# Kernel tuning notes

Measured on AMD Instinct MI355X. Metric: run time of the kernel, lower is better.

Reference implementation:

```python
import jax, jax.numpy as jnp
import numpy as np

TAPS = 5
DELAY = 3
EPS_POWER = 1e-7   # clamp for inverse power (wpe_one_iteration eps)
EPS_REG = 1e-10    # diagonal loading of the correlation matrix


def setup_inputs() -> dict:
    key = jax.random.key(0)
    ks = jax.random.split(key, 5)
    B, F, C, T = 8, 257, 8, 800
    shp = (B, F, C, T)
    return {
        "data_sep_real": jax.random.normal(ks[0], shp, jnp.float32),
        "data_sep_imag": jax.random.normal(ks[1], shp, jnp.float32),
        "data_mix_real": jax.random.normal(ks[2], shp, jnp.float32),
        "data_mix_imag": jax.random.normal(ks[3], shp, jnp.float32),
        "ilens": jax.random.randint(ks[4], (B,), 1, T + 1, jnp.int32),
    }


def _ytilde(Y, taps, delay):
    # Y: (B,F,C,T) complex -> stacked delayed taps (B,F,taps*C,T)
    # tap k at time t holds Y[..., t - delay - k] (zero-padded past)
    B, F, C, T = Y.shape
    Yp = jnp.pad(Y, ((0, 0), (0, 0), (0, 0), (delay + taps - 1, 0)))
    tilde = jnp.stack(
        [Yp[..., taps - 1 - k: taps - 1 - k + T] for k in range(taps)], axis=2
    )  # (B,F,taps,C,T)
    return tilde.reshape(B, F, taps * C, T)


def _wpe_one_iteration(Y, power, taps, delay):
    # Y: (B,F,C,T) complex, power: (B,F,T) real
    B, F, C, T = Y.shape
    inv_power = 1.0 / jnp.maximum(power, EPS_POWER)          # (B,F,T)
    Yt = _ytilde(Y, taps, delay)                              # (B,F,K,T), K=taps*C
    t0 = delay + taps - 1                                     # correlations use t >= t0
    Ytv = Yt[..., t0:]
    Yv = Y[..., t0:]
    Ytw = Ytv * inv_power[:, :, None, t0:].astype(Y.dtype)
    # R = sum_t w(t) Ytilde(t) Ytilde(t)^H  -> (B,F,K,K)
    R = jnp.einsum('bfat,bfct->bfac', Ytw, jnp.conj(Ytv))
    # P = sum_t w(t) Ytilde(t) Y(t)^H      -> (B,F,K,C)
    P = jnp.einsum('bfat,bfet->bfae', Ytw, jnp.conj(Yv))
    K = taps * C
    R = R + EPS_REG * jnp.eye(K, dtype=R.dtype)
    G = jnp.linalg.solve(R, P)                                # (B,F,K,C)
    # X(t) = Y(t) - G^H Ytilde(t)
    X = Y - jnp.einsum('bfae,bfat->bfet', jnp.conj(G), Yt)
    return X


def reference(data_sep_real, data_sep_imag, data_mix_real, data_mix_imag, ilens):
    # power of separated signal, averaged over channels (use_dnn_mask=False)
    power = jnp.mean(data_sep_real ** 2 + data_sep_imag ** 2, axis=-2)  # (B,F,T)
    Ym = jax.lax.complex(data_mix_real, data_mix_imag)                  # (B,F,C,T)
    X = _wpe_one_iteration(Ym, power, TAPS, DELAY)
    # zero out padded frames: t >= ilens[b]
    t = jnp.arange(X.shape[-1])
    valid = t[None, :] < ilens[:, None]                                 # (B,T)
    X = jnp.where(valid[:, None, None, :], X, 0)
    # return real/imag stacked on last axis: (B,F,C,T,2)
    return jnp.stack([X.real, X.imag], axis=-1)
```

## Files before the change

### kernel.cpp

```cpp
#include <hip/hip_runtime.h>

#define B 8
#define F 257
#define C 8
#define T 800
#define TAPS 5
#define DELAY 3
#define K 40
#define NCOL 48
#define T0 7
#define BF (B*F)

typedef __bf16 bf16x8 __attribute__((ext_vector_type(8)));
typedef __bf16 bf16x4 __attribute__((ext_vector_type(4)));
typedef float f32x4 __attribute__((ext_vector_type(4)));

struct PF { float4 v[3]; };

__global__ __launch_bounds__(256) void power_kernel(const float* __restrict__ sr,
                                                    const float* __restrict__ si,
                                                    float* __restrict__ W) {
    int bf = blockIdx.x;
    const float* srp = sr + (size_t)bf * C * T;
    const float* sip = si + (size_t)bf * C * T;
    int t0 = threadIdx.x * 4;
    if (t0 < T) {
        float s[4] = {0.f, 0.f, 0.f, 0.f};
#pragma unroll
        for (int c = 0; c < C; ++c) {
            float4 a = *(const float4*)(srp + c * T + t0);
            float4 b = *(const float4*)(sip + c * T + t0);
            s[0] = fmaf(a.x, a.x, fmaf(b.x, b.x, s[0]));
            s[1] = fmaf(a.y, a.y, fmaf(b.y, b.y, s[1]));
            s[2] = fmaf(a.z, a.z, fmaf(b.z, b.z, s[2]));
            s[3] = fmaf(a.w, a.w, fmaf(b.w, b.w, s[3]));
        }
        float4 w;
        float* wp = (float*)&w;
#pragma unroll
        for (int e = 0; e < 4; ++e) {
            float v = fmaxf(s[e] * (1.0f / C), 1e-7f);
            wp[e] = (t0 + e < T0) ? 0.f : rsqrtf(v);
        }
        *(float4*)(W + (size_t)bf * T + t0) = w;
    }
}

#define WB 10624

__global__ __launch_bounds__(256, 3) void rp_mfma_kernel(const float* __restrict__ mr,
                                                         const float* __restrict__ mi,
                                                         const float* __restrict__ W,
                                                         float2* __restrict__ Rout,
                                                         float2* __restrict__ Pout) {
    __shared__ __align__(16) unsigned char SH[4 * WB];
    const int lane = threadIdx.x & 63;
    const int wid = threadIdx.x >> 6;
    const int bf = blockIdx.x * 4 + wid;
    unsigned char* base = SH + wid * WB;
    float* sre = (float*)(base + 7680);
    float* sim_ = (float*)(base + 9088);
    float* wsh = (float*)(base + 10496);

    const float* mrp = mr + (size_t)bf * C * T;
    const float* mip = mi + (size_t)bf * C * T;
    const float* Wp  = W  + (size_t)bf * T;

    const int q = lane >> 4, col = lane & 15;
    const int pc = lane >> 3, pg = lane & 7;

    const int PM[6] = {0, 0, 0, 1, 1, 2};
    const int PN[6] = {0, 1, 2, 1, 2, 2};

    f32x4 accRe[6], accIr[6], accRi[6];
#pragma unroll
    for (int p = 0; p < 6; ++p) {
        accRe[p] = (f32x4){0.f, 0.f, 0.f, 0.f};
        accIr[p] = (f32x4){0.f, 0.f, 0.f, 0.f};
        accRi[p] = (f32x4){0.f, 0.f, 0.f, 0.f};
    }

    for (int ks = 0; ks < 25; ++ks) {
        const int tb = ks * 32;

#pragma unroll
        for (int it = 0; it < 3; ++it) {
            int task = lane + it * 64;
            if (task < 160) {
                int pl = task / 80;
                int rem = task - pl * 80;
                int c = rem / 10, grp = rem - c * 10;
                int tg = tb - 8 + grp * 4;
                const float* srcp = pl ? mip : mrp;
                float4 v = make_float4(0.f, 0.f, 0.f, 0.f);
                if (tg >= 0) v = *(const float4*)(srcp + c * T + tg);
                *(float4*)((pl ? sim_ : sre) + c * 44 + grp * 4) = v;
            } else if (task < 168) {
                int grp = task - 160;
                *(float4*)(wsh + grp * 4) = *(const float4*)(Wp + tb + grp * 4);
            }
        }

        {
            int ybase = pc * 44 + pg * 4;
            float yre[12], yim[12];
            float4 r0 = *(const float4*)(sre + ybase);
            float4 r1 = *(const float4*)(sre + ybase + 4);
            float4 r2 = *(const float4*)(sre + ybase + 8);
            float4 i0 = *(const float4*)(sim_ + ybase);
            float4 i1 = *(const float4*)(sim_ + ybase + 4);
            float4 i2 = *(const float4*)(sim_ + ybase + 8);
            yre[0] = r0.x; yre[1] = r0.y; yre[2]  = r0.z; yre[3]  = r0.w;
            yre[4] = r1.x; yre[5] = r1.y; yre[6]  = r1.z; yre[7]  = r1.w;
            yre[8] = r2.x; yre[9] = r2.y; yre[10] = r2.z; yre[11] = r2.w;
            yim[0] = i0.x; yim[1] = i0.y; yim[2]  = i0.z; yim[3]  = i0.w;
            yim[4] = i1.x; yim[5] = i1.y; yim[6]  = i1.z; yim[7]  = i1.w;
            yim[8] = i2.x; yim[9] = i2.y; yim[10] = i2.z; yim[11] = i2.w;
            float4 w4 = *(const float4*)(wsh + pg * 4);
            float wv[4] = {w4.x, w4.y, w4.z, w4.w};
#pragma unroll
            for (int v = 0; v < 6; ++v) {
                int row = (v < 5) ? (v * 8 + pc) : (40 + pc);
                int off = (v < 5) ? (5 - v) : 8;
                bf16x4 zr, zi;
#pragma unroll
                for (int e = 0; e < 4; ++e) {
                    zr[e] = (__bf16)(wv[e] * yre[off + e]);
                    zi[e] = (__bf16)(wv[e] * yim[off + e]);
                }
                *(bf16x4*)(base + row * 80 + pg * 8) = zr;
                *(bf16x4*)(base + 3840 + row * 80 + pg * 8) = zi;
            }
        }

        bf16x8 fr[3], fi[3];
#pragma unroll
        for (int X = 0; X < 3; ++X) {
            fr[X] = *(const bf16x8*)(base + (X * 16 + col) * 80 + q * 16);
            fi[X] = *(const bf16x8*)(base + 3840 + (X * 16 + col) * 80 + q * 16);
        }
#pragma unroll
        for (int p = 0; p < 6; ++p) {
            int mt = PM[p], nt = PN[p];
            accRe[p] = __builtin_amdgcn_mfma_f32_16x16x32_bf16(fr[mt], fr[nt], accRe[p], 0, 0, 0);
            accRe[p] = __builtin_amdgcn_mfma_f32_16x16x32_bf16(fi[mt], fi[nt], accRe[p], 0, 0, 0);
            accIr[p] = __builtin_amdgcn_mfma_f32_16x16x32_bf16(fi[mt], fr[nt], accIr[p], 0, 0, 0);
            accRi[p] = __builtin_amdgcn_mfma_f32_16x16x32_bf16(fr[mt], fi[nt], accRi[p], 0, 0, 0);
        }
    }

    float2* Rp = Rout + (size_t)bf * K * K;
    float2* Pp = Pout + (size_t)bf * K * C;
#pragma unroll
    for (int p = 0; p < 6; ++p) {
        int mt = PM[p], nt = PN[p];
#pragma unroll
        for (int r = 0; r < 4; ++r) {
            int m = mt * 16 + q * 4 + r;
            int n = nt * 16 + col;
            float re = accRe[p][r];
            float im = accIr[p][r] - accRi[p][r];
            if (m < K) {
                if (n < K) {
                    if (m == n) re += 1e-10f;
                    Rp[m * K + n] = make_float2(re, im);
                } else {
                    Pp[m * C + (n - K)] = make_float2(re, im);
                }
            }
            if (mt != nt && m < K && n < K)
                Rp[n * K + m] = make_float2(re, -im);
        }
    }
}

__device__ __forceinline__ float rdlane(float v, int j) {
    return __uint_as_float(__builtin_amdgcn_readlane(__float_as_uint(v), (unsigned)j));
}

__global__ __launch_bounds__(64, 2) void solve_kernel(const float2* __restrict__ Rin,
                                                      const float2* __restrict__ Pin,
                                                      float2* __restrict__ Gout) {
    const int bf = blockIdx.x;
    const int lane = threadIdx.x;
    const bool act = lane < K;

    float2 row[NCOL];
    {
        const float4* Rp4 = (const float4*)(Rin + (size_t)bf * K * K + (size_t)(act ? lane : 0) * K);
        const float4* Pp4 = (const float4*)(Pin + (size_t)bf * K * C + (size_t)(act ? lane : 0) * C);
#pragma unroll
        for (int m = 0; m < K / 2; ++m) {
            float4 v = Rp4[m];
            if (!act) v = make_float4(0.f, 0.f, 0.f, 0.f);
            row[2 * m]     = make_float2(v.x, v.y);
            row[2 * m + 1] = make_float2(v.z, v.w);
        }
#pragma unroll
        for (int m = 0; m < C / 2; ++m) {
            float4 v = Pp4[m];
            if (!act) v = make_float4(0.f, 0.f, 0.f, 0.f);
            row[K + 2 * m]     = make_float2(v.x, v.y);
            row[K + 2 * m + 1] = make_float2(v.z, v.w);
        }
    }

#pragma unroll
    for (int j = 0; j < K; ++j) {
        float dx = rdlane(row[j].x, j);
        float dy = rdlane(row[j].y, j);
        float den = fmaf(dx, dx, dy * dy);
        float r = 1.0f / den;
        float ix = dx * r;
        float iy = -dy * r;
        float lx = row[j].x * ix - row[j].y * iy;
        float ly = row[j].x * iy + row[j].y * ix;
        bool isj = (lane == j);
        lx = isj ? (1.0f - ix) : lx;
        ly = isj ? (0.0f - iy) : ly;
#pragma unroll
        for (int n = j; n < NCOL; ++n) {
            float ux = rdlane(row[n].x, j);
            float uy = rdlane(row[n].y, j);
            row[n].x = fmaf(-lx, ux, fmaf( ly, uy, row[n].x));
            row[n].y = fmaf(-lx, uy, fmaf(-ly, ux, row[n].y));
        }
    }

    if (act) {
        float4* Gp = (float4*)(Gout + (size_t)bf * K * C + (size_t)lane * C);
#pragma unroll
        for (int m = 0; m < C / 2; ++m)
            Gp[m] = make_float4(row[K + 2 * m].x, row[K + 2 * m].y,
                                row[K + 2 * m + 1].x, row[K + 2 * m + 1].y);
    }
}

#define XSTR 144
#define XWB 12032

__device__ __forceinline__ PF x_load(const float* __restrict__ mrp,
                                     const float* __restrict__ mip,
                                     int tb, int lane) {
    PF p;
#pragma unroll
    for (int it = 0; it < 3; ++it) {
        int task = lane + it * 64;
        float4 v = make_float4(0.f, 0.f, 0.f, 0.f);
        if (task < 160) {
            int pl = task / 80;
            int rem = task - pl * 80;
            int c = rem / 10, grp = rem - c * 10;
            int tg = tb - 8 + grp * 4;
            const float* srcp = pl ? mip : mrp;
            if (tg >= 0) v = *(const float4*)(srcp + c * T + tg);
        }
        p.v[it] = v;
    }
    return p;
}

__device__ __forceinline__ void x_store(const PF& p, float* sre, float* sim_, int lane) {
#pragma unroll
    for (int it = 0; it < 3; ++it) {
        int task = lane + it * 64;
        if (task < 160) {
            int pl = task / 80;
            int rem = task - pl * 80;
            int c = rem / 10, grp = rem - c * 10;
            *(float4*)((pl ? sim_ : sre) + c * 44 + grp * 4) = p.v[it];
        }
    }
}

__global__ __launch_bounds__(64) void x_mfma_kernel(const float* __restrict__ mr,
                                                    const float* __restrict__ mi,
                                                    const float2* __restrict__ Gin,
                                                    const int* __restrict__ ilens,
                                                    float2* __restrict__ out) {
    __shared__ __align__(16) unsigned char SH[XWB];
    const int lane = threadIdx.x;
    const int gid = blockIdx.x;
    const int bf = gid >> 2;
    const int split = gid & 3;
    const int ck0 = (split == 0) ? 0 : (1 + split * 6);
    const int nck = (split == 0) ? 7 : 6;
    unsigned char* base = SH;
    float* sre = (float*)(base + 9216);
    float* sim_ = (float*)(base + 10624);

    const float* mrp = mr + (size_t)bf * C * T;
    const float* mip = mi + (size_t)bf * C * T;
    const float2* Gp = Gin + (size_t)bf * K * C;
    float2* outp = out + (size_t)bf * C * T;
    const int len = ilens[bf / F];

    const int q = lane >> 4, col = lane & 15;
    const int t2 = lane >> 1, half = lane & 1;

#pragma unroll
    for (int pl = 0; pl < 2; ++pl) {
        unsigned char* pb = base + pl * 4608 + t2 * XSTR + 80 + half * 24;
        *(float2*)(pb)      = make_float2(0.f, 0.f);
        *(float2*)(pb + 8)  = make_float2(0.f, 0.f);
        *(float2*)(pb + 16) = make_float2(0.f, 0.f);
    }

    bf16x8 Agr[2], Agi[2], Agin[2];
#pragma unroll
    for (int ks = 0; ks < 2; ++ks)
#pragma unroll
        for (int j = 0; j < 8; ++j) {
            int a = ks * 32 + q * 8 + j;
            float2 g = make_float2(0.f, 0.f);
            if (a < K && col < C) g = Gp[a * C + col];
            Agr[ks][j]  = (__bf16)g.x;
            Agi[ks][j]  = (__bf16)g.y;
            Agin[ks][j] = (__bf16)(-g.y);
        }

    PF cur = x_load(mrp, mip, ck0 * 32, lane);

    for (int ci = 0; ci < nck; ++ci) {
        const int tb = (ck0 + ci) * 32;

        x_store(cur, sre, sim_, lane);
        if (ci + 1 < nck) cur = x_load(mrp, mip, tb + 32, lane);

#pragma unroll
        for (int i = 0; i < 5; ++i) {
            int abase = half * 20 + 4 * i;
            bf16x4 zr, zi;
#pragma unroll
            for (int e2 = 0; e2 < 4; ++e2) {
                int a = abase + e2;
                int v = a >> 3, c = a & 7;
                int idx = c * 44 + t2 + 5 - v;
                zr[e2] = (__bf16)sre[idx];
                zi[e2] = (__bf16)sim_[idx];
            }
            *(bf16x4*)(base + t2 * XSTR + abase * 2) = zr;
            *(bf16x4*)(base + 4608 + t2 * XSTR + abase * 2) = zi;
        }

#pragma unroll
        for (int tt = 0; tt < 2; ++tt) {
            const int trow = tt * 16 + col;
            f32x4 accRe = (f32x4){0.f, 0.f, 0.f, 0.f};
            f32x4 accIm = (f32x4){0.f, 0.f, 0.f, 0.f};
#pragma unroll
            for (int ks = 0; ks < 2; ++ks) {
                bf16x8 byr = *(const bf16x8*)(base + trow * XSTR + ks * 64 + q * 16);
                bf16x8 byi = *(const bf16x8*)(base + 4608 + trow * XSTR + ks * 64 + q * 16);
                accRe = __builtin_amdgcn_mfma_f32_16x16x32_bf16(Agr[ks], byr, accRe, 0, 0, 0);
                accRe = __builtin_amdgcn_mfma_f32_16x16x32_bf16(Agi[ks], byi, accRe, 0, 0, 0);
                accIm = __builtin_amdgcn_mfma_f32_16x16x32_bf16(Agr[ks], byi, accIm, 0, 0, 0);
                accIm = __builtin_amdgcn_mfma_f32_16x16x32_bf16(Agin[ks], byr, accIm, 0, 0, 0);
            }
            if (q < 2) {
                int t = tb + tt * 16 + col;
                int l = tt * 16 + col + 8;
                bool ok = (t < len);
#pragma unroll
                for (int r = 0; r < 4; ++r) {
                    int e = q * 4 + r;
                    float yr = sre[e * 44 + l];
                    float yi = sim_[e * 44 + l];
                    float2 v = ok ? make_float2(yr - accRe[r], yi - accIm[r])
                                  : make_float2(0.f, 0.f);
                    outp[e * T + t] = v;
                }
            }
        }
    }
}

extern "C" void kernel_launch(void* const* d_in, const int* in_sizes, int n_in,
                              void* d_out, int out_size, void* d_ws, size_t ws_size,
                              hipStream_t stream) {
    const float* sep_r = (const float*)d_in[0];
    const float* sep_i = (const float*)d_in[1];
    const float* mix_r = (const float*)d_in[2];
    const float* mix_i = (const float*)d_in[3];
    const int* ilens   = (const int*)d_in[4];

    float* ws = (float*)d_ws;
    float* W = ws;
    float2* Rws = (float2*)(ws + (size_t)BF * T);
    float2* Gws = Rws + (size_t)BF * K * K;

    power_kernel<<<BF, 256, 0, stream>>>(sep_r, sep_i, W);
    rp_mfma_kernel<<<BF / 4, 256, 0, stream>>>(mix_r, mix_i, W, Rws, Gws);
    solve_kernel<<<BF, 64, 0, stream>>>(Rws, Gws, Gws);
    x_mfma_kernel<<<BF * 4, 64, 0, stream>>>(mix_r, mix_i, Gws, ilens, (float2*)d_out);
}
```

Before: 187.0 us.

## Double-buffer mixture staging with async global_load_lds DMA prefetch

Replaces the synchronous per-step global-to-register-to-LDS staging of the mixture real/imag tiles and weights with global_load_lds direct-to-LDS copies into two alternating buffers. The copy for step k+1 is issued before the compute of step k, so load latency is meant to overlap with MFMA work. The halo at the start is zero-filled manually. LDS per block grows and launch bounds drop from 3 to 2 blocks per CU, which reduces occupancy. The slot layout changes from 44-float rows to 160-byte rows.

```diff
diff --git a/kernel.cpp b/kernel.cpp
--- a/kernel.cpp
+++ b/kernel.cpp
@@ -17,6 +17,12 @@
 
 struct PF { float4 v[3]; };
 
+__device__ __forceinline__ void dma16(const void* g, void* l) {
+    __builtin_amdgcn_global_load_lds(
+        (const __attribute__((address_space(1))) void*)g,
+        (__attribute__((address_space(3))) void*)l, 16, 0, 0);
+}
+
 __global__ __launch_bounds__(256) void power_kernel(const float* __restrict__ sr,
                                                     const float* __restrict__ si,
                                                     float* __restrict__ W) {
@@ -46,21 +52,20 @@
     }
 }
 
-#define WB 10624
-
-__global__ __launch_bounds__(256, 3) void rp_mfma_kernel(const float* __restrict__ mr,
+#define WB2 13824
+
+__global__ __launch_bounds__(256, 2) void rp_mfma_kernel(const float* __restrict__ mr,
                                                          const float* __restrict__ mi,
                                                          const float* __restrict__ W,
                                                          float2* __restrict__ Rout,
                                                          float2* __restrict__ Pout) {
-    __shared__ __align__(16) unsigned char SH[4 * WB];
+    __shared__ __align__(16) unsigned char SH[4 * WB2];
     const int lane = threadIdx.x & 63;
     const int wid = threadIdx.x >> 6;
     const int bf = blockIdx.x * 4 + wid;
-    unsigned char* base = SH + wid * WB;
-    float* sre = (float*)(base + 7680);
-    float* sim_ = (float*)(base + 9088);
-    float* wsh = (float*)(base + 10496);
+    unsigned char* base = SH + wid * WB2;
+    unsigned char* b0 = base + 7680;
+    unsigned char* b1 = base + 10752;
 
     const float* mrp = mr + (size_t)bf * C * T;
     const float* mip = mi + (size_t)bf * C * T;
@@ -71,6 +76,29 @@
 
     const int PM[6] = {0, 0, 0, 1, 1, 2};
     const int PN[6] = {0, 1, 2, 1, 2, 2};
+
+    const float* sb[3];
+    const float* sb0[3];
+    bool hal[3];
+#pragma unroll
+    for (int it = 0; it < 3; ++it) {
+        int task = lane + it * 64;
+        hal[it] = false;
+        if (task < 160) {
+            int row = task / 10, grp = task - row * 10;
+            int pl = row >> 3, c = row & 7;
+            const float* cb = (pl ? mip : mrp) + c * T;
+            sb[it] = cb + grp * 4 - 8;
+            hal[it] = (grp < 2);
+            sb0[it] = hal[it] ? cb : sb[it];
+        } else if (task < 168) {
+            sb[it] = Wp + (task - 160) * 4;
+            sb0[it] = sb[it];
+        } else {
+            sb[it] = mrp + (task - 168) * 4;
+            sb0[it] = sb[it];
+        }
+    }
 
     f32x4 accRe[6], accIr[6], accRi[6];
 #pragma unroll
@@ -80,43 +108,45 @@
         accRi[p] = (f32x4){0.f, 0.f, 0.f, 0.f};
     }
 
+#pragma unroll
+    for (int it = 0; it < 3; ++it)
+        dma16(sb0[it], b0 + (lane + it * 64) * 16);
+    asm volatile("s_waitcnt vmcnt(0)" ::: "memory");
+#pragma unroll
+    for (int it = 0; it < 3; ++it) {
+        int task = lane + it * 64;
+        if (hal[it])
+            *(float4*)(b0 + task * 16) = make_float4(0.f, 0.f, 0.f, 0.f);
+    }
+    __builtin_amdgcn_sched_barrier(0);
+
     for (int ks = 0; ks < 25; ++ks) {
-        const int tb = ks * 32;
-
-#pragma unroll
-        for (int it = 0; it < 3; ++it) {
-            int task = lane + it * 64;
-            if (task < 160) {
-                int pl = task / 80;
-                int rem = task - pl * 80;
-                int c = rem / 10, grp = rem - c * 10;
-                int tg = tb - 8 + grp * 4;
-                const float* srcp = pl ? mip : mrp;
-                float4 v = make_float4(0.f, 0.f, 0.f, 0.f);
-                if (tg >= 0) v = *(const float4*)(srcp + c * T + tg);
-                *(float4*)((pl ? sim_ : sre) + c * 44 + grp * 4) = v;
-            } else if (task < 168) {
-                int grp = task - 160;
-                *(float4*)(wsh + grp * 4) = *(const float4*)(Wp + tb + grp * 4);
-            }
-        }
+        unsigned char* buf = (ks & 1) ? b1 : b0;
+        unsigned char* nbuf = (ks & 1) ? b0 : b1;
+        int ntb = (ks < 24) ? (ks + 1) * 32 : ks * 32;
+#pragma unroll
+        for (int it = 0; it < 3; ++it)
+            dma16(sb[it] + ntb, nbuf + (lane + it * 64) * 16);
+        asm volatile("s_waitcnt vmcnt(3)" ::: "memory");
+        __builtin_amdgcn_sched_barrier(0);
 
         {
-            int ybase = pc * 44 + pg * 4;
+            const float* yrr = (const float*)(buf + pc * 160);
+            const float* yir = (const float*)(buf + (8 + pc) * 160);
             float yre[12], yim[12];
-            float4 r0 = *(const float4*)(sre + ybase);
-            float4 r1 = *(const float4*)(sre + ybase + 4);
-            float4 r2 = *(const float4*)(sre + ybase + 8);
-            float4 i0 = *(const float4*)(sim_ + ybase);
-            float4 i1 = *(const float4*)(sim_ + ybase + 4);
-            float4 i2 = *(const float4*)(sim_ + ybase + 8);
+            float4 r0 = *(const float4*)(yrr + pg * 4);
+            float4 r1 = *(const float4*)(yrr + pg * 4 + 4);
+            float4 r2 = *(const float4*)(yrr + pg * 4 + 8);
+            float4 i0 = *(const float4*)(yir + pg * 4);
+            float4 i1 = *(const float4*)(yir + pg * 4 + 4);
+            float4 i2 = *(const float4*)(yir + pg * 4 + 8);
             yre[0] = r0.x; yre[1] = r0.y; yre[2]  = r0.z; yre[3]  = r0.w;
             yre[4] = r1.x; yre[5] = r1.y; yre[6]  = r1.z; yre[7]  = r1.w;
             yre[8] = r2.x; yre[9] = r2.y; yre[10] = r2.z; yre[11] = r2.w;
             yim[0] = i0.x; yim[1] = i0.y; yim[2]  = i0.z; yim[3]  = i0.w;
             yim[4] = i1.x; yim[5] = i1.y; yim[6]  = i1.z; yim[7]  = i1.w;
             yim[8] = i2.x; yim[9] = i2.y; yim[10] = i2.z; yim[11] = i2.w;
-            float4 w4 = *(const float4*)(wsh + pg * 4);
+            float4 w4 = *(const float4*)(buf + 2560 + pg * 16);
             float wv[4] = {w4.x, w4.y, w4.z, w4.w};
 #pragma unroll
             for (int v = 0; v < 6; ++v) {
```

Result: faster. 181.3 us (-3.1%).
